# Kernel tuning notes

Hardware: AMD Instinct MI355X
Metric: run time of the kernel (lower is better)

## Reference

```python
import jax, jax.numpy as jnp
import numpy as np

S = 128          # spatial grid size per axis
N = 100000       # active voxels
C_IN = 32
C_OUT = 32
FS = 3           # filter size per axis -> 27 offsets


def _build_rulebook():
    """Build submanifold-conv rulebook: for each active site and each of the
    27 filter offsets, the index of the active neighbor (or masked out)."""
    rng = np.random.default_rng(0)
    coords = rng.integers(0, S, size=(2 * N, 3))
    lin = coords[:, 0] * S * S + coords[:, 1] * S + coords[:, 2]
    lin = np.unique(lin)[:N]                      # sorted unique active sites
    xyz = np.stack([lin // (S * S), (lin // S) % S, lin % S], axis=1)  # [N,3]
    offs = np.stack(np.meshgrid(*([np.arange(FS) - FS // 2] * 3), indexing='ij'), -1).reshape(-1, 3)  # [27,3]
    nb = xyz[:, None, :] + offs[None, :, :]       # [N,27,3]
    inb = np.all((nb >= 0) & (nb < S), axis=-1)   # in-bounds
    nb_lin = nb[..., 0] * S * S + nb[..., 1] * S + nb[..., 2]
    pos = np.searchsorted(lin, nb_lin)
    pos_c = np.clip(pos, 0, N - 1)
    found = inb & (lin[pos_c] == nb_lin)
    nbr_idx = np.where(found, pos_c, 0).astype(np.int32)   # [N,27]
    return nbr_idx, found


def setup_inputs() -> dict:
    key = jax.random.key(0)
    k1, k2 = jax.random.split(key)
    nbr_idx, nbr_mask = _build_rulebook()
    K = FS ** 3
    std = (2.0 / C_IN / K) ** 0.5   # matches module init
    return {
        'features': jax.random.normal(k1, (N, C_IN), dtype=jnp.float32),
        'weight': std * jax.random.normal(k2, (K, C_IN, C_OUT), dtype=jnp.float32),
        'bias': jnp.zeros((C_OUT,), dtype=jnp.float32),
        'nbr_idx': jnp.asarray(nbr_idx),
        'nbr_mask': jnp.asarray(nbr_mask),
    }


def reference(features, weight, bias, nbr_idx, nbr_mask):
    # Submanifold sparse conv: gather active neighbors per filter offset,
    # multiply by per-offset [Cin,Cout] weight, accumulate at active sites.
    gathered = jnp.where(nbr_mask[:, :, None], features[nbr_idx], 0.0)  # [N,K,Cin]
    out = jnp.einsum('nki,kio->no', gathered, weight) + bias            # [N,Cout]
    return out
```

## Files before the change

### kernel.cpp

```cpp
#include <hip/hip_runtime.h>
#include <hip/hip_bf16.h>

#define NVOX 100000
#define CIN 32
#define COUT 32
#define KOFF 27

typedef __attribute__((ext_vector_type(8))) short short8;
typedef __attribute__((ext_vector_type(4))) float float4v;
typedef __attribute__((ext_vector_type(4))) int   int4v;

__device__ __forceinline__ short f2bf(float x) {
    union { float f; unsigned u; } v; v.f = x;
    unsigned u = v.u;
    u += 0x7FFFu + ((u >> 16) & 1u);
    return (short)(u >> 16);
}

__global__ __launch_bounds__(256) void feat_cvt_kernel(
    const float* __restrict__ feat, unsigned short* __restrict__ fbf)
{
    int i = (blockIdx.x * 256 + threadIdx.x) * 4;
    if (i < NVOX * CIN) {
        float4v f = *(const float4v*)(feat + i);
        short s[4] = { f2bf(f.x), f2bf(f.y), f2bf(f.z), f2bf(f.w) };
        *(ulonglong1*)(fbf + i) = *(ulonglong1*)s;
    } else if (i < (NVOX + 1) * CIN) {
        short s[4] = { 0, 0, 0, 0 };
        *(ulonglong1*)(fbf + i) = *(ulonglong1*)s;
    }
}

__global__ __launch_bounds__(256) void wgt_cvt_kernel(
    const float* __restrict__ weight, short8* __restrict__ wfrag)
{
    int g = blockIdx.x * 256 + threadIdx.x;
    if (g >= KOFF * 2 * 64) return;
    int k   = g >> 7;
    int rem = g & 127;
    int t   = rem >> 6;
    int ln  = rem & 63;
    int co  = t * 16 + (ln & 15);
    int cib = (ln >> 4) * 8;
    const float* wp = weight + (k * CIN + cib) * COUT + co;
    short8 b;
#pragma unroll
    for (int j = 0; j < 8; ++j) b[j] = f2bf(wp[j * COUT]);
    wfrag[g] = b;
}

__global__ __launch_bounds__(256) void enc_fold_kernel(
    const int* __restrict__ nbr_idx, const int* __restrict__ nbr_mask,
    int* __restrict__ enc)
{
    int i = (blockIdx.x * 256 + threadIdx.x) * 4;
    if (i >= NVOX * KOFF) return;
    int4v id = *(const int4v*)(nbr_idx + i);
    int4v mk = *(const int4v*)(nbr_mask + i);
    int4v e;
    e.x = mk.x ? id.x : NVOX;
    e.y = mk.y ? id.y : NVOX;
    e.z = mk.z ? id.z : NVOX;
    e.w = mk.w ? id.w : NVOX;
    *(int4v*)(enc + i) = e;
}

__global__ __launch_bounds__(1024, 8) void subm_conv_kernel(
    const unsigned short* __restrict__ fbf,
    const short8* __restrict__ wfrag,
    const float* __restrict__ bias,
    const int* __restrict__ enc_g,
    float* __restrict__ out)
{
    __shared__ short8 wlds[KOFF * 2 * 64];

    const int tid  = threadIdx.x;
    const int lane = tid & 63;
    const int wave = tid >> 6;
    const int m    = lane & 15;
    const int quad = lane >> 4;

    const int v0 = (blockIdx.x * 16 + wave) * 16;
    int v = v0 + m;
    if (v > NVOX - 1) v = NVOX - 1;

    const int* ep = enc_g + v * KOFF;
    int enc[KOFF];
#pragma unroll
    for (int k = 0; k < KOFF; ++k) enc[k] = ep[k];

    for (int g = tid; g < KOFF * 2 * 64; g += 1024) wlds[g] = wfrag[g];
    __syncthreads();

    float4v acc0 = {0.f, 0.f, 0.f, 0.f};
    float4v acc1 = {0.f, 0.f, 0.f, 0.f};

    const char* fb = (const char*)fbf;
    const int   boff = quad * 16;

    short8 abuf[4];
#pragma unroll
    for (int k = 0; k < 4; ++k)
        abuf[k] = *(const short8*)(fb + (size_t)enc[k] * 64 + boff);

#pragma unroll
    for (int k = 0; k < KOFF; ++k) {
        const int slot = k & 3;
        short8 a = abuf[slot];
        if (k + 4 < KOFF)
            abuf[slot] = *(const short8*)(fb + (size_t)enc[k + 4] * 64 + boff);

        short8 wb0 = wlds[k * 128 + lane];
        short8 wb1 = wlds[k * 128 + 64 + lane];
        acc0 = __builtin_amdgcn_mfma_f32_16x16x32_bf16(a, wb0, acc0, 0, 0, 0);
        acc1 = __builtin_amdgcn_mfma_f32_16x16x32_bf16(a, wb1, acc1, 0, 0, 0);
    }

    const float bs0 = bias[m];
    const float bs1 = bias[16 + m];
#pragma unroll
    for (int r = 0; r < 4; ++r) {
        int vv = v0 + quad * 4 + r;
        if (vv < NVOX) {
            out[(size_t)vv * COUT + m]      = acc0[r] + bs0;
            out[(size_t)vv * COUT + 16 + m] = acc1[r] + bs1;
        }
    }
}

extern "C" void kernel_launch(void* const* d_in, const int* in_sizes, int n_in,
                              void* d_out, int out_size, void* d_ws, size_t ws_size,
                              hipStream_t stream) {
    const float* feat = (const float*)d_in[0];
    const float* wgt  = (const float*)d_in[1];
    const float* bias = (const float*)d_in[2];
    const int*   nidx = (const int*)d_in[3];
    const int*   nmsk = (const int*)d_in[4];
    float*       out  = (float*)d_out;

    unsigned short* fbf   = (unsigned short*)d_ws;
    short8*         wfrag = (short8*)((char*)d_ws + 6400064);
    int*            enc   = (int*)((char*)d_ws + 6400064 + 55296);

    feat_cvt_kernel<<<((NVOX + 1) * CIN / 4 + 255) / 256, 256, 0, stream>>>(feat, fbf);
    wgt_cvt_kernel<<<(KOFF * 2 * 64 + 255) / 256, 256, 0, stream>>>(wgt, wfrag);
    enc_fold_kernel<<<(NVOX * KOFF / 4 + 255) / 256, 256, 0, stream>>>(nidx, nmsk, enc);

    const int block = 1024;
    const int grid  = (NVOX + 255) / 256;
    subm_conv_kernel<<<grid, block, 0, stream>>>(fbf, wfrag, bias, enc, out);
}
```

Measured before the change: 105.9 us.

## Pad neighbor table to 28, prescale offsets, deepen gather prefetch, shrink blocks

The neighbor-index table is padded from 27 to 28 entries per voxel and stored pre-shifted by 64, so each row is read as seven 16-byte vector loads and no multiply is needed when forming gather addresses. The gather prefetch ring grows from 4 to 8 slots to keep more feature loads in flight. The conv kernel moves from 1024-thread to 512-thread blocks. The fold kernel now uses one thread per entry with 64 lanes per voxel, so 36 of every 64 threads sit idle, and the deeper prefetch raises register pressure.

```diff
diff --git a/kernel.cpp b/kernel.cpp
--- a/kernel.cpp
+++ b/kernel.cpp
@@ -5,6 +5,7 @@
 #define CIN 32
 #define COUT 32
 #define KOFF 27
+#define KPAD 28
 
 typedef __attribute__((ext_vector_type(8))) short short8;
 typedef __attribute__((ext_vector_type(4))) float float4v;
@@ -51,25 +52,27 @@
 
 __global__ __launch_bounds__(256) void enc_fold_kernel(
     const int* __restrict__ nbr_idx, const int* __restrict__ nbr_mask,
-    int* __restrict__ enc)
+    int* __restrict__ encb)
 {
-    int i = (blockIdx.x * 256 + threadIdx.x) * 4;
-    if (i >= NVOX * KOFF) return;
-    int4v id = *(const int4v*)(nbr_idx + i);
-    int4v mk = *(const int4v*)(nbr_mask + i);
-    int4v e;
-    e.x = mk.x ? id.x : NVOX;
-    e.y = mk.y ? id.y : NVOX;
-    e.z = mk.z ? id.z : NVOX;
-    e.w = mk.w ? id.w : NVOX;
-    *(int4v*)(enc + i) = e;
+    int v = blockIdx.x * 4 + (threadIdx.x >> 6);
+    int k = threadIdx.x & 63;
+    if (v >= NVOX || k >= KPAD) return;
+    int e;
+    if (k < KOFF) {
+        int id = nbr_idx[v * KOFF + k];
+        int mk = nbr_mask[v * KOFF + k];
+        e = (mk ? id : NVOX) << 6;
+    } else {
+        e = NVOX << 6;
+    }
+    encb[v * KPAD + k] = e;
 }
 
-__global__ __launch_bounds__(1024, 8) void subm_conv_kernel(
+__global__ __launch_bounds__(512, 4) void subm_conv_kernel(
     const unsigned short* __restrict__ fbf,
     const short8* __restrict__ wfrag,
     const float* __restrict__ bias,
-    const int* __restrict__ enc_g,
+    const int* __restrict__ encb,
     float* __restrict__ out)
 {
     __shared__ short8 wlds[KOFF * 2 * 64];
@@ -80,35 +83,36 @@
     const int m    = lane & 15;
     const int quad = lane >> 4;
 
-    const int v0 = (blockIdx.x * 16 + wave) * 16;
+    const int v0 = (blockIdx.x * 8 + wave) * 16;
     int v = v0 + m;
     if (v > NVOX - 1) v = NVOX - 1;
 
-    const int* ep = enc_g + v * KOFF;
-    int enc[KOFF];
+    const int4v* ep = (const int4v*)(encb + v * KPAD);
+    int4v encv[7];
 #pragma unroll
-    for (int k = 0; k < KOFF; ++k) enc[k] = ep[k];
+    for (int q = 0; q < 7; ++q) encv[q] = ep[q];
+    const int* enc = (const int*)encv;
 
-    for (int g = tid; g < KOFF * 2 * 64; g += 1024) wlds[g] = wfrag[g];
+    for (int g = tid; g < KOFF * 2 * 64; g += 512) wlds[g] = wfrag[g];
     __syncthreads();
 
     float4v acc0 = {0.f, 0.f, 0.f, 0.f};
     float4v acc1 = {0.f, 0.f, 0.f, 0.f};
 
-    const char* fb = (const char*)fbf;
+    const char* fb  = (const char*)fbf;
     const int   boff = quad * 16;
 
-    short8 abuf[4];
+    short8 abuf[8];
 #pragma unroll
-    for (int k = 0; k < 4; ++k)
-        abuf[k] = *(const short8*)(fb + (size_t)enc[k] * 64 + boff);
+    for (int k = 0; k < 8; ++k)
+        abuf[k] = *(const short8*)(fb + (size_t)(unsigned)enc[k] + boff);
 
 #pragma unroll
     for (int k = 0; k < KOFF; ++k) {
-        const int slot = k & 3;
+        const int slot = k & 7;
         short8 a = abuf[slot];
-        if (k + 4 < KOFF)
-            abuf[slot] = *(const short8*)(fb + (size_t)enc[k + 4] * 64 + boff);
+        if (k + 8 < KOFF)
+            abuf[slot] = *(const short8*)(fb + (size_t)(unsigned)enc[k + 8] + boff);
 
         short8 wb0 = wlds[k * 128 + lane];
         short8 wb1 = wlds[k * 128 + 64 + lane];
@@ -140,13 +144,13 @@
 
     unsigned short* fbf   = (unsigned short*)d_ws;
     short8*         wfrag = (short8*)((char*)d_ws + 6400064);
-    int*            enc   = (int*)((char*)d_ws + 6400064 + 55296);
+    int*            encb  = (int*)((char*)d_ws + 6400064 + 55296);
 
     feat_cvt_kernel<<<((NVOX + 1) * CIN / 4 + 255) / 256, 256, 0, stream>>>(feat, fbf);
     wgt_cvt_kernel<<<(KOFF * 2 * 64 + 255) / 256, 256, 0, stream>>>(wgt, wfrag);
-    enc_fold_kernel<<<(NVOX * KOFF / 4 + 255) / 256, 256, 0, stream>>>(nidx, nmsk, enc);
+    enc_fold_kernel<<<(NVOX + 3) / 4, 256, 0, stream>>>(nidx, nmsk, encb);
 
-    const int block = 1024;
-    const int grid  = (NVOX + 255) / 256;
-    subm_conv_kernel<<<grid, block, 0, stream>>>(fbf, wfrag, bias, enc, out);
+    const int block = 512;
+    const int grid  = (NVOX + 127) / 128;
+    subm_conv_kernel<<<grid, block, 0, stream>>>(fbf, wfrag, bias, encb, out);
 }
```

Result: slower. 115.7 us (+9.3%).
